# Optimization experiments

Hardware: AMD Instinct MI355X
Metric: run time of the kernel (lower is better)

## Reference

```python
import jax, jax.numpy as jnp
import numpy as np

NUM_EXPERTS = 8
TOP_K = 2
RANK = 16
LORA_ALPHA = 32
SCALING = LORA_ALPHA / RANK  # 2.0


def setup_inputs() -> dict:
    key = jax.random.key(0)
    ks = jax.random.split(key, 6)
    B, S, D_IN, D_OUT = 4, 2048, 4096, 4096
    x = jax.random.normal(ks[0], (B, S, D_IN), dtype=jnp.float32)
    W_base = jax.random.normal(ks[1], (D_OUT, D_IN), dtype=jnp.float32) * 0.02
    b_base = jax.random.normal(ks[2], (D_OUT,), dtype=jnp.float32) * 0.02
    W_router = jax.random.normal(ks[3], (NUM_EXPERTS, D_IN), dtype=jnp.float32) * 0.02
    A = jax.random.normal(ks[4], (NUM_EXPERTS, RANK, D_IN), dtype=jnp.float32) * 0.02
    Bm = jax.random.normal(ks[5], (D_OUT, RANK), dtype=jnp.float32) * 0.02
    Bm = jnp.broadcast_to(Bm, (NUM_EXPERTS, D_OUT, RANK)) * jnp.arange(1, NUM_EXPERTS + 1, dtype=jnp.float32)[:, None, None] * 0.2
    return {"x": x, "W_base": W_base, "b_base": b_base, "W_router": W_router, "A": A, "B": Bm}


def reference(x, W_base, b_base, W_router, A, B):
    bs, seq, d_in = x.shape
    T = bs * seq
    xf = x.reshape(T, d_in)  # flatten tokens, as in torch .view(-1, d_in)

    # base linear layer
    base = xf @ W_base.T + b_base  # [T, d_out]

    # local router: logits -> top-k -> softmax over selected weights
    logits = xf @ W_router.T                      # [T, E]
    rw, sel = jax.lax.top_k(logits, TOP_K)        # [T, K] each
    rw = jax.nn.softmax(rw, axis=-1)              # router_norm == 'softmax'

    # per-token per-expert combine weight (zero for unselected experts);
    # mathematically identical to gather-LoRA-scatter since top-k experts
    # per token are distinct.
    onehot = jax.nn.one_hot(sel, NUM_EXPERTS, dtype=rw.dtype)  # [T, K, E]
    w = jnp.einsum('tk,tke->te', rw, onehot)                   # [T, E]

    # LoRA: down-project to tiny rank, weight, then up-project; contract
    # expert+rank together to avoid a [T, E, d_out] intermediate.
    h = jnp.einsum('td,erd->ter', xf, A)          # [T, E, r] (small)
    lora = jnp.einsum('ter,te,eor->to', h, w, B) * SCALING  # [T, d_out]

    return (base + lora).reshape(bs, seq, -1)
```

## Files before the change

kernel.cpp:

```cpp
#include <hip/hip_runtime.h>
#include <hip/hip_bf16.h>
#include <stdint.h>

#define T_TOKENS 8192
#define DIN      4096
#define DOUT     4096
#define NE       8
#define RANK     16
#define KEXT     128
#define KTOT     4224
#define SCALING  2.0f

typedef __attribute__((ext_vector_type(8))) short   short8;
typedef __attribute__((ext_vector_type(4))) float   float4v;

__device__ __forceinline__ unsigned short f2bf(float f) {
    union { float f; unsigned int u; } c; c.f = f;
    unsigned int u = c.u;
    u += 0x7FFFu + ((u >> 16) & 1u);
    return (unsigned short)(u >> 16);
}

#define GLD_LDS(g, l) __builtin_amdgcn_global_load_lds( \
    (const __attribute__((address_space(1))) void*)(g), \
    (__attribute__((address_space(3))) void*)(l), 16, 0, 0)

__global__ __launch_bounds__(256) void k_front(const float* __restrict__ x,
                                               const float* __restrict__ Wr,
                                               const float* __restrict__ Wb,
                                               const float* __restrict__ A,
                                               const float* __restrict__ Bm,
                                               unsigned short* __restrict__ xa,
                                               unsigned short* __restrict__ Wa,
                                               unsigned short* __restrict__ Acat,
                                               float* __restrict__ w8) {
    __shared__ float lds_wr[8 * 1024];
    int b = blockIdx.x;
    int tid = threadIdx.x;

    if (b < 2048) {
        int l = tid & 63, w = tid >> 6;
        int t = b * 4 + w;
        const float4* x4 = (const float4*)x;
        const float4* Wr4 = (const float4*)Wr;
        unsigned short* xarow = xa + (size_t)t * KTOT;

        float racc[NE];
#pragma unroll
        for (int e = 0; e < NE; e++) racc[e] = 0.f;

        for (int ci = 0; ci < 4; ci++) {
            __syncthreads();
#pragma unroll
            for (int jj = 0; jj < 8; jj++) {
                int f = jj * 256 + tid;
                int e = f >> 8, col = f & 255;
                *(float4*)&lds_wr[f * 4] = Wr4[e * 1024 + ci * 256 + col];
            }
            __syncthreads();
            float4 xv[4];
#pragma unroll
            for (int j = 0; j < 4; j++)
                xv[j] = x4[(size_t)t * 1024 + ci * 256 + j * 64 + l];
#pragma unroll
            for (int j = 0; j < 4; j++) {
                ushort4 p;
                p.x = f2bf(xv[j].x); p.y = f2bf(xv[j].y);
                p.z = f2bf(xv[j].z); p.w = f2bf(xv[j].w);
                *(ushort4*)(xarow + (ci * 256 + j * 64 + l) * 4) = p;
            }
#pragma unroll
            for (int e = 0; e < NE; e++) {
#pragma unroll
                for (int j = 0; j < 4; j++) {
                    float4 wv = *(const float4*)&lds_wr[(e * 256 + j * 64 + l) * 4];
                    racc[e] += xv[j].x * wv.x + xv[j].y * wv.y + xv[j].z * wv.z + xv[j].w * wv.w;
                }
            }
        }
#pragma unroll
        for (int e = 0; e < NE; e++) {
            float v = racc[e];
#pragma unroll
            for (int off = 32; off > 0; off >>= 1) v += __shfl_xor(v, off);
            racc[e] = v;
        }
        if (l == 0) {
            int e0 = 0;
#pragma unroll
            for (int e = 1; e < NE; e++) if (racc[e] > racc[e0]) e0 = e;
            int e1 = -1;
#pragma unroll
            for (int e = 0; e < NE; e++)
                if (e != e0 && (e1 < 0 || racc[e] > racc[e1])) e1 = e;
            float a1 = __expf(racc[e1] - racc[e0]);
            float inv = 1.0f / (1.0f + a1);
            float* wrow = w8 + t * NE;
#pragma unroll
            for (int e = 0; e < NE; e++)
                wrow[e] = (e == e0) ? inv * SCALING : ((e == e1) ? a1 * inv * SCALING : 0.f);
        }
    } else if (b < 18432) {
        int idx = (b - 2048) * 256 + tid;
        float4 v = ((const float4*)Wb)[idx];
        int o  = idx >> 10;
        int kc = idx & 1023;
        ushort4 p;
        p.x = f2bf(v.x); p.y = f2bf(v.y); p.z = f2bf(v.z); p.w = f2bf(v.w);
        *(ushort4*)(Wa + (size_t)o * KTOT + kc * 4) = p;
    } else {
        int tid2 = (b - 18432) * 256 + tid;
        if (tid2 < NE * RANK * DIN) {
            Acat[tid2] = f2bf(A[tid2]);
        } else {
            int j   = tid2 - NE * RANK * DIN;
            int o   = j >> 7;
            int rem = j & 127;
            int e   = rem >> 4;
            int r   = rem & 15;
            Wa[(size_t)o * KTOT + DIN + rem] = f2bf(Bm[(size_t)e * (DOUT * RANK) + o * RANK + r]);
        }
    }
}

__global__ __launch_bounds__(256) void k_h(unsigned short* __restrict__ xa,
                                           const unsigned short* __restrict__ Acat,
                                           const float* __restrict__ w8) {
    __shared__ unsigned short lds_x[32 * 128];
    __shared__ unsigned short lds_a[128 * 128];
    int m0  = blockIdx.x * 32;
    int tid = threadIdx.x;
    int l = tid & 63, w = tid >> 6;
    int quad = l >> 4, lr = l & 15;

    float4v acc[2][2] = {};

    for (int k0 = 0; k0 < DIN; k0 += 128) {
        __syncthreads();
#pragma unroll
        for (int it = 0; it < 2; it++) {
            int c = it * 256 + tid;
            int row = c >> 4, s = c & 15;
            int kc = s ^ (row & 15);
            GLD_LDS(xa + (size_t)(m0 + row) * KTOT + k0 + kc * 8, lds_x + c * 8);
        }
#pragma unroll
        for (int it = 0; it < 8; it++) {
            int c = it * 256 + tid;
            int row = c >> 4, s = c & 15;
            int kc = s ^ (row & 15);
            GLD_LDS(Acat + (size_t)row * DIN + k0 + kc * 8, lds_a + c * 8);
        }
        __syncthreads();
#pragma unroll
        for (int kk = 0; kk < 4; kk++) {
            int kc = kk * 4 + quad;
            short8 a[2], bfr[2];
#pragma unroll
            for (int mi = 0; mi < 2; mi++) {
                int row = mi * 16 + lr;
                a[mi] = *(const short8*)&lds_x[row * 128 + ((kc ^ lr) * 8)];
            }
#pragma unroll
            for (int ni = 0; ni < 2; ni++) {
                int row = w * 32 + ni * 16 + lr;
                bfr[ni] = *(const short8*)&lds_a[row * 128 + ((kc ^ lr) * 8)];
            }
#pragma unroll
            for (int mi = 0; mi < 2; mi++)
#pragma unroll
                for (int ni = 0; ni < 2; ni++)
                    acc[mi][ni] = __builtin_amdgcn_mfma_f32_16x16x32_bf16(a[mi], bfr[ni], acc[mi][ni], 0, 0, 0);
        }
    }

#pragma unroll
    for (int mi = 0; mi < 2; mi++)
#pragma unroll
        for (int ni = 0; ni < 2; ni++) {
            int col = w * 32 + ni * 16 + lr;
            int e = col >> 4;
#pragma unroll
            for (int i = 0; i < 4; i++) {
                int t = m0 + mi * 16 + quad * 4 + i;
                float v = acc[mi][ni][i] * w8[t * NE + e];
                xa[(size_t)t * KTOT + DIN + col] = f2bf(v);
            }
        }
}

__global__ __launch_bounds__(256) void k_main(const unsigned short* __restrict__ xa,
                                              const unsigned short* __restrict__ Wa,
                                              const float* __restrict__ bias,
                                              float* __restrict__ out) {
    __shared__ unsigned short lds[2 * 128 * 32];
    int bm = blockIdx.x, bn = blockIdx.y;
    int tid = threadIdx.x;
    int l = tid & 63, w = tid >> 6;
    int quad = l >> 4, lr = l & 15;
    int wm = w >> 1, wn = w & 1;

    const size_t xbase = (size_t)bm * 128 * KTOT;
    const size_t wbase = (size_t)bn * 128 * KTOT;

    float4v acc[4][4] = {};

    for (int k0 = 0; k0 < KTOT; k0 += 32) {
        __syncthreads();
#pragma unroll
        for (int it = 0; it < 2; it++) {
            int c = it * 256 + tid;
            int row = c >> 2, kc = c & 3;
            GLD_LDS(xa + xbase + (size_t)row * KTOT + k0 + kc * 8, lds + c * 8);
            GLD_LDS(Wa + wbase + (size_t)row * KTOT + k0 + kc * 8, lds + 4096 + c * 8);
        }
        __syncthreads();

        short8 a[4], b[4];
#pragma unroll
        for (int mi = 0; mi < 4; mi++)
            a[mi] = *(const short8*)(lds + (wm * 64 + mi * 16 + lr) * 32 + quad * 8);
#pragma unroll
        for (int ni = 0; ni < 4; ni++)
            b[ni] = *(const short8*)(lds + 4096 + (wn * 64 + ni * 16 + lr) * 32 + quad * 8);
#pragma unroll
        for (int mi = 0; mi < 4; mi++)
#pragma unroll
            for (int ni = 0; ni < 4; ni++)
                acc[mi][ni] = __builtin_amdgcn_mfma_f32_16x16x32_bf16(a[mi], b[ni], acc[mi][ni], 0, 0, 0);
    }

    int trow0 = bm * 128 + wm * 64;
    int ocol0 = bn * 128 + wn * 64;
#pragma unroll
    for (int ni = 0; ni < 4; ni++) {
        int o = ocol0 + ni * 16 + lr;
        float bb = bias[o];
#pragma unroll
        for (int mi = 0; mi < 4; mi++) {
#pragma unroll
            for (int i = 0; i < 4; i++) {
                int t = trow0 + mi * 16 + quad * 4 + i;
                out[(size_t)t * DOUT + o] = acc[mi][ni][i] + bb;
            }
        }
    }
}

extern "C" void kernel_launch(void* const* d_in, const int* in_sizes, int n_in,
                              void* d_out, int out_size, void* d_ws, size_t ws_size,
                              hipStream_t stream) {
    const float* x  = (const float*)d_in[0];
    const float* Wb = (const float*)d_in[1];
    const float* bb = (const float*)d_in[2];
    const float* Wr = (const float*)d_in[3];
    const float* A  = (const float*)d_in[4];
    const float* Bm = (const float*)d_in[5];
    float* out = (float*)d_out;

    char* ws = (char*)d_ws;
    unsigned short* xa   = (unsigned short*)(ws);
    unsigned short* Wa   = (unsigned short*)(ws + 69206016);
    unsigned short* Acat = (unsigned short*)(ws + 69206016 + 34603008);
    float*          w8   = (float*)(ws + 69206016 + 34603008 + 1048576);

    k_front<<<dim3(22528), dim3(256), 0, stream>>>(x, Wr, Wb, A, Bm, xa, Wa, Acat, w8);
    k_h    <<<dim3(256),   dim3(256), 0, stream>>>(xa, Acat, w8);
    k_main <<<dim3(64, 32), dim3(256), 0, stream>>>(xa, Wa, bb, out);
}
```

Baseline: 632.6 us.

## Rewrite main GEMM with 256x256 tiles, double-buffered LDS pipeline and swizzle

Replaces the 128x128 single-buffered GEMM with a 512-thread, 256x256-tile kernel that uses 128KB of dynamic LDS, double-buffered K=64 stages and direct global-to-LDS prefetch interleaved with MFMA phases. It adds an XOR swizzle on the LDS layout to avoid bank conflicts, a block-index remap for L2 locality, and s_setprio around the MFMA bursts. The aim is to hide global load latency and raise arithmetic intensity per LDS byte. The cost is much more LDS per block and higher register pressure, which limits occupancy, plus hand-tuned waitcnt and barrier logic that is fragile.

```diff
diff --git a/kernel.cpp b/kernel.cpp
--- a/kernel.cpp
+++ b/kernel.cpp
@@ -9,6 +9,7 @@
 #define RANK     16
 #define KEXT     128
 #define KTOT     4224
+#define NT       66
 #define SCALING  2.0f
 
 typedef __attribute__((ext_vector_type(8))) short   short8;
@@ -189,59 +190,111 @@
         }
 }
 
-__global__ __launch_bounds__(256) void k_main(const unsigned short* __restrict__ xa,
-                                              const unsigned short* __restrict__ Wa,
-                                              const float* __restrict__ bias,
-                                              float* __restrict__ out) {
-    __shared__ unsigned short lds[2 * 128 * 32];
-    int bm = blockIdx.x, bn = blockIdx.y;
+#define LOADA(dst, basep, mlo) { \
+    _Pragma("unroll") for (int i_ = 0; i_ < 4; i_++) \
+        dst[i_] = *(const short8*)((basep) + aoff + ((mlo) + i_) * 1024); }
+#define LOADB(dst, basep) { \
+    _Pragma("unroll") for (int i_ = 0; i_ < 4; i_++) \
+        dst[i_] = *(const short8*)((basep) + boff + i_ * 1024); }
+#define MFMA44(mlo) { \
+    __builtin_amdgcn_s_setprio(1); \
+    _Pragma("unroll") for (int i_ = 0; i_ < 4; i_++) \
+    _Pragma("unroll") for (int j_ = 0; j_ < 4; j_++) \
+        acc[(mlo) + i_][j_] = __builtin_amdgcn_mfma_f32_16x16x32_bf16(af[i_], bf[j_], acc[(mlo) + i_][j_], 0, 0, 0); \
+    __builtin_amdgcn_s_setprio(0); }
+#define STAGE(srcP, regbase, ts, kh, tb) do { \
+    const unsigned short* s_ = (srcP) + (size_t)((ts) * 64 + (kh) * 32); \
+    char* d_ = smem + (regbase) + (tb) * 32768 + (kh) * 16384 + tid16; \
+    GLD_LDS(s_, d_); \
+    GLD_LDS(s_ + (size_t)128 * KTOT, d_ + 8192); \
+} while (0)
+#define BAR() __builtin_amdgcn_s_barrier()
+#define LGKM0() do { asm volatile("s_waitcnt lgkmcnt(0)" ::: "memory"); \
+                     __builtin_amdgcn_sched_barrier(0); } while (0)
+
+__global__ __launch_bounds__(512, 2) void k_main(const unsigned short* __restrict__ xa,
+                                                 const unsigned short* __restrict__ Wa,
+                                                 const float* __restrict__ bias,
+                                                 float* __restrict__ out) {
+    extern __shared__ char smem[];
     int tid = threadIdx.x;
     int l = tid & 63, w = tid >> 6;
-    int quad = l >> 4, lr = l & 15;
-    int wm = w >> 1, wn = w & 1;
-
-    const size_t xbase = (size_t)bm * 128 * KTOT;
-    const size_t wbase = (size_t)bn * 128 * KTOT;
-
-    float4v acc[4][4] = {};
-
-    for (int k0 = 0; k0 < KTOT; k0 += 32) {
-        __syncthreads();
-#pragma unroll
-        for (int it = 0; it < 2; it++) {
-            int c = it * 256 + tid;
-            int row = c >> 2, kc = c & 3;
-            GLD_LDS(xa + xbase + (size_t)row * KTOT + k0 + kc * 8, lds + c * 8);
-            GLD_LDS(Wa + wbase + (size_t)row * KTOT + k0 + kc * 8, lds + 4096 + c * 8);
-        }
-        __syncthreads();
-
-        short8 a[4], b[4];
-#pragma unroll
-        for (int mi = 0; mi < 4; mi++)
-            a[mi] = *(const short8*)(lds + (wm * 64 + mi * 16 + lr) * 32 + quad * 8);
-#pragma unroll
-        for (int ni = 0; ni < 4; ni++)
-            b[ni] = *(const short8*)(lds + 4096 + (wn * 64 + ni * 16 + lr) * 32 + quad * 8);
-#pragma unroll
-        for (int mi = 0; mi < 4; mi++)
-#pragma unroll
-            for (int ni = 0; ni < 4; ni++)
-                acc[mi][ni] = __builtin_amdgcn_mfma_f32_16x16x32_bf16(a[mi], b[ni], acc[mi][ni], 0, 0, 0);
-    }
-
-    int trow0 = bm * 128 + wm * 64;
-    int ocol0 = bn * 128 + wn * 64;
+    int lr = l & 15, quad = l >> 4;
+    int wm = w >> 2, wn = w & 3;
+
+    int bid = blockIdx.x;
+    int wg  = (bid & 7) * 64 + (bid >> 3);
+    int bm  = wg & 31, bn = wg >> 5;
+
+    int laneoff = (lr * 4 + (quad ^ ((lr >> 1) & 3))) * 16;
+    int aoff = wm * 8192 + laneoff;
+    int boff = wn * 4096 + laneoff;
+
+    int srow  = w * 16 + ((tid >> 2) & 15);
+    int skq   = (tid & 3) ^ ((tid >> 3) & 3);
+    int tid16 = tid * 16;
+    const unsigned short* srcA = xa + (size_t)(bm * 256 + srow) * KTOT + skq * 8;
+    const unsigned short* srcB = Wa + (size_t)(bn * 256 + srow) * KTOT + skq * 8;
+
+    float4v acc[8][4] = {};
+    short8 af[4], bf[4];
+
+    STAGE(srcA, 0,     0, 0, 0);
+    STAGE(srcB, 65536, 0, 0, 0);
+    STAGE(srcA, 0,     0, 1, 0);
+    STAGE(srcB, 65536, 0, 1, 0);
+    STAGE(srcA, 0,     1, 0, 1);
+    STAGE(srcB, 65536, 1, 0, 1);
+    asm volatile("s_waitcnt vmcnt(4)" ::: "memory");
+    BAR();
+
+    for (int t = 0; t < NT; ++t) {
+        int buf  = t & 1, nbuf = buf ^ 1;
+        int ts1  = (t + 1 < NT) ? t + 1 : NT - 1;
+        int ts2  = (t + 2 < NT) ? t + 2 : NT - 1;
+        const char* pa = smem + buf * 32768;
+        const char* pb = smem + 65536 + buf * 32768;
+
+        LOADA(af, pa, 0);
+        LOADB(bf, pb);
+        STAGE(srcA, 0, ts1, 1, nbuf);
+        BAR(); LGKM0();
+        MFMA44(0);
+        BAR();
+
+        LOADA(af, pa, 4);
+        STAGE(srcB, 65536, ts1, 1, nbuf);
+        BAR(); LGKM0();
+        MFMA44(4);
+        BAR();
+
+        LOADA(af, pa + 16384, 0);
+        LOADB(bf, pb + 16384);
+        STAGE(srcA, 0, ts2, 0, buf);
+        BAR(); LGKM0();
+        MFMA44(0);
+        BAR();
+
+        LOADA(af, pa + 16384, 4);
+        STAGE(srcB, 65536, ts2, 0, buf);
+        asm volatile("s_waitcnt vmcnt(4)" ::: "memory");
+        BAR(); LGKM0();
+        MFMA44(4);
+        BAR();
+    }
+
+    int trow0 = bm * 256 + wm * 128;
+    int ocol0 = bn * 256 + wn * 64;
 #pragma unroll
     for (int ni = 0; ni < 4; ni++) {
         int o = ocol0 + ni * 16 + lr;
         float bb = bias[o];
 #pragma unroll
-        for (int mi = 0; mi < 4; mi++) {
+        for (int mi = 0; mi < 8; mi++) {
 #pragma unroll
             for (int i = 0; i < 4; i++) {
-                int t = trow0 + mi * 16 + quad * 4 + i;
-                out[(size_t)t * DOUT + o] = acc[mi][ni][i] + bb;
+                int trow = trow0 + mi * 16 + quad * 4 + i;
+                out[(size_t)trow * DOUT + o] = acc[mi][ni][i] + bb;
             }
         }
     }
@@ -264,7 +317,14 @@
     unsigned short* Acat = (unsigned short*)(ws + 69206016 + 34603008);
     float*          w8   = (float*)(ws + 69206016 + 34603008 + 1048576);
 
+    static bool attr_done = false;
+    if (!attr_done) {
+        hipFuncSetAttribute((const void*)k_main,
+                            hipFuncAttributeMaxDynamicSharedMemorySize, 131072);
+        attr_done = true;
+    }
+
     k_front<<<dim3(22528), dim3(256), 0, stream>>>(x, Wr, Wb, A, Bm, xa, Wa, Acat, w8);
     k_h    <<<dim3(256),   dim3(256), 0, stream>>>(xa, Acat, w8);
-    k_main <<<dim3(64, 32), dim3(256), 0, stream>>>(xa, Wa, bb, out);
-}
+    k_main <<<dim3(512),   dim3(512), 131072, stream>>>(xa, Wa, bb, out);
+}
```

After: 571.3 us. 1.11x faster.

## Restructure main GEMM with 256x128 tiles, double-buffered LDS, swizzle and XCD mapping

Applied to the files above, without the earlier changes.

Rewrites the main bf16 GEMM kernel to use 512-thread blocks on 256x128 output tiles. Global-to-LDS loads are issued two stages ahead into a double buffer, with explicit vmcnt/lgkmcnt waits replacing full syncthreads. LDS layout is XOR-swizzled to cut bank conflicts, and block IDs are remapped per XCD so tiles sharing operands stay in the same L2. MFMA sections raise wave priority. The intent is to overlap memory with compute and improve operand reuse, at the cost of fragile hand-tuned wait counts and higher LDS use per block.

```diff
diff --git a/kernel.cpp b/kernel.cpp
--- a/kernel.cpp
+++ b/kernel.cpp
@@ -9,6 +9,7 @@
 #define RANK     16
 #define KEXT     128
 #define KTOT     4224
+#define NS       132
 #define SCALING  2.0f
 
 typedef __attribute__((ext_vector_type(8))) short   short8;
@@ -189,48 +190,79 @@
         }
 }
 
-__global__ __launch_bounds__(256) void k_main(const unsigned short* __restrict__ xa,
-                                              const unsigned short* __restrict__ Wa,
-                                              const float* __restrict__ bias,
-                                              float* __restrict__ out) {
-    __shared__ unsigned short lds[2 * 128 * 32];
-    int bm = blockIdx.x, bn = blockIdx.y;
+#define BAR() __builtin_amdgcn_s_barrier()
+#define LGKM0() do { asm volatile("s_waitcnt lgkmcnt(0)" ::: "memory"); \
+                     __builtin_amdgcn_sched_barrier(0); } while (0)
+#define STAGEA6(ts, b) do { \
+    const unsigned short* s_ = srcA + (size_t)(ts) * 32; \
+    char* d_ = smem + (b) * 16384 + tid16; \
+    GLD_LDS(s_, d_); \
+    GLD_LDS(s_ + (size_t)128 * KTOT, d_ + 8192); \
+} while (0)
+#define STAGEB6(ts, b) do { \
+    const unsigned short* s_ = srcB + (size_t)(ts) * 32; \
+    char* d_ = smem + 32768 + (b) * 8192 + tid16; \
+    GLD_LDS(s_, d_); \
+} while (0)
+
+__global__ __launch_bounds__(512, 4) void k_main(const unsigned short* __restrict__ xa,
+                                                 const unsigned short* __restrict__ Wa,
+                                                 const float* __restrict__ bias,
+                                                 float* __restrict__ out) {
+    __shared__ __align__(16) char smem[49152];
     int tid = threadIdx.x;
     int l = tid & 63, w = tid >> 6;
-    int quad = l >> 4, lr = l & 15;
+    int lr = l & 15, quad = l >> 4;
     int wm = w >> 1, wn = w & 1;
 
-    const size_t xbase = (size_t)bm * 128 * KTOT;
-    const size_t wbase = (size_t)bn * 128 * KTOT;
+    int bid = blockIdx.x;
+    int xcd = bid & 7, idx = bid >> 3;
+    int bm  = (xcd & 3) * 8 + (idx & 7);
+    int bn  = (xcd >> 2) * 16 + (idx >> 3);
+
+    int laneoff = lr * 64 + ((quad ^ ((lr >> 1) & 3)) << 4);
+    int amioff = wm * 4096 + laneoff;
+    int bnioff = wn * 4096 + laneoff;
+
+    int srow  = w * 16 + ((tid >> 2) & 15);
+    int skq   = (tid & 3) ^ ((tid >> 3) & 3);
+    int tid16 = tid * 16;
+    const unsigned short* srcA = xa + (size_t)(bm * 256 + srow) * KTOT + skq * 8;
+    const unsigned short* srcB = Wa + (size_t)(bn * 128 + srow) * KTOT + skq * 8;
 
     float4v acc[4][4] = {};
-
-    for (int k0 = 0; k0 < KTOT; k0 += 32) {
-        __syncthreads();
-#pragma unroll
-        for (int it = 0; it < 2; it++) {
-            int c = it * 256 + tid;
-            int row = c >> 2, kc = c & 3;
-            GLD_LDS(xa + xbase + (size_t)row * KTOT + k0 + kc * 8, lds + c * 8);
-            GLD_LDS(Wa + wbase + (size_t)row * KTOT + k0 + kc * 8, lds + 4096 + c * 8);
-        }
-        __syncthreads();
-
-        short8 a[4], b[4];
+    short8 af[4], bf[4];
+
+    STAGEA6(0, 0); STAGEB6(0, 0);
+    STAGEA6(1, 1); STAGEB6(1, 1);
+
+    for (int s = 0; s < NS; ++s) {
+        int b = s & 1;
+        asm volatile("s_waitcnt vmcnt(3)" ::: "memory");
+        BAR();
+        const char* pa = smem + b * 16384;
+        const char* pb = smem + 32768 + b * 8192;
 #pragma unroll
         for (int mi = 0; mi < 4; mi++)
-            a[mi] = *(const short8*)(lds + (wm * 64 + mi * 16 + lr) * 32 + quad * 8);
+            af[mi] = *(const short8*)(pa + amioff + mi * 1024);
 #pragma unroll
         for (int ni = 0; ni < 4; ni++)
-            b[ni] = *(const short8*)(lds + 4096 + (wn * 64 + ni * 16 + lr) * 32 + quad * 8);
+            bf[ni] = *(const short8*)(pb + bnioff + ni * 1024);
+        LGKM0();
+        BAR();
+        int ts2 = (s + 2 < NS) ? s + 2 : NS - 1;
+        STAGEA6(ts2, b); STAGEB6(ts2, b);
+        __builtin_amdgcn_s_setprio(1);
 #pragma unroll
         for (int mi = 0; mi < 4; mi++)
 #pragma unroll
             for (int ni = 0; ni < 4; ni++)
-                acc[mi][ni] = __builtin_amdgcn_mfma_f32_16x16x32_bf16(a[mi], b[ni], acc[mi][ni], 0, 0, 0);
+                acc[mi][ni] = __builtin_amdgcn_mfma_f32_16x16x32_bf16(af[mi], bf[ni], acc[mi][ni], 0, 0, 0);
+        __builtin_amdgcn_s_setprio(0);
     }
-
-    int trow0 = bm * 128 + wm * 64;
+    asm volatile("s_waitcnt vmcnt(0) lgkmcnt(0)" ::: "memory");
+
+    int trow0 = bm * 256 + wm * 64;
     int ocol0 = bn * 128 + wn * 64;
 #pragma unroll
     for (int ni = 0; ni < 4; ni++) {
@@ -240,8 +272,8 @@
         for (int mi = 0; mi < 4; mi++) {
 #pragma unroll
             for (int i = 0; i < 4; i++) {
-                int t = trow0 + mi * 16 + quad * 4 + i;
-                out[(size_t)t * DOUT + o] = acc[mi][ni][i] + bb;
+                int trow = trow0 + mi * 16 + quad * 4 + i;
+                out[(size_t)trow * DOUT + o] = acc[mi][ni][i] + bb;
             }
         }
     }
@@ -266,5 +298,5 @@
 
     k_front<<<dim3(22528), dim3(256), 0, stream>>>(x, Wr, Wb, A, Bm, xa, Wa, Acat, w8);
     k_h    <<<dim3(256),   dim3(256), 0, stream>>>(xa, Acat, w8);
-    k_main <<<dim3(64, 32), dim3(256), 0, stream>>>(xa, Wa, bb, out);
-}
+    k_main <<<dim3(1024),  dim3(512), 0, stream>>>(xa, Wa, bb, out);
+}
```

New measurement: 587.7 us. 7.1% less time.
